# Kernel optimization log

Measured on AMD Instinct MI355X. Metric: run time of the kernel, lower is better.

The kernel has to match this reference:

```python
import jax, jax.numpy as jnp
import numpy as np

B, T, D, H = 2, 2048, 1024, 16
DK = D // H


def setup_inputs() -> dict:
    key = jax.random.key(0)
    ks = jax.random.split(key, 12)
    q = jax.random.normal(ks[0], (B, T, D), jnp.float32)
    k = jax.random.normal(ks[1], (B, T, D), jnp.float32)
    v = jax.random.normal(ks[2], (B, T, D), jnp.float32)
    # padding mask [B,1,T]: 1 = valid, 0 = pad (nonzero per torch eq(0) semantics)
    lengths = jnp.array([T, (3 * T) // 4])
    mask = (jnp.arange(T)[None, None, :] < lengths[:, None, None]).astype(jnp.int32)
    s = 0.02
    Wq = jax.random.normal(ks[3], (D, D), jnp.float32) * s
    Wk = jax.random.normal(ks[4], (D, D), jnp.float32) * s
    Wv = jax.random.normal(ks[5], (D, D), jnp.float32) * s
    Wo = jax.random.normal(ks[6], (D, D), jnp.float32) * s
    bq = jnp.zeros((D,), jnp.float32)
    bk = jnp.zeros((D,), jnp.float32)
    bv = jnp.zeros((D,), jnp.float32)
    bo = jnp.zeros((D,), jnp.float32)
    return {"query": q, "key": k, "value": v, "mask": mask,
            "Wq": Wq, "bq": bq, "Wk": Wk, "bk": bk,
            "Wv": Wv, "bv": bv, "Wo": Wo, "bo": bo}


def reference(query, key, value, mask, Wq, bq, Wk, bk, Wv, bv, Wo, bo):
    # q,k,v projections -> [B, H, T, DK]
    def proj(x, W, b):
        return (x @ W.T + b).reshape(B, T, H, DK).transpose(0, 2, 1, 3)
    q = proj(query, Wq, bq)
    k = proj(key, Wk, bk)
    v = proj(value, Wv, bv)
    scores = jnp.einsum("bhqd,bhkd->bhqk", q, k) * (DK ** -0.5)  # [B,H,T,T]
    m = (mask == 0)[:, None, :, :]  # [B,1,1,T] broadcast over heads/queries
    scores = jnp.where(m, -jnp.inf, scores)
    attn = jax.nn.softmax(scores, axis=-1)
    attn = jnp.where(m, 0.0, attn)
    x = jnp.einsum("bhqk,bhkd->bhqd", attn, v)  # [B,H,T,DK]
    x = x.transpose(0, 2, 1, 3).reshape(B, T, D)
    return x @ Wo.T + bo
```

## Files before the change

### kernel.cpp

```cpp
#include <hip/hip_runtime.h>

typedef unsigned short u16;
typedef unsigned int u32;
typedef __bf16 bf16x8 __attribute__((ext_vector_type(8)));
typedef __bf16 bf16x4 __attribute__((ext_vector_type(4)));
typedef float floatx4 __attribute__((ext_vector_type(4)));

#define BB 2
#define TT 2048
#define DD 1024
#define HH 16
#define DKK 64
#define ACT (BB * TT * DD)
#define WTE (DD * DD)

__device__ inline u16 f2bf(float f) {
    union { float f; u32 u; } c; c.f = f;
    u32 r = (c.u + 0x7fffu + ((c.u >> 16) & 1u)) >> 16;
    return (u16)r;
}
__device__ inline u32 pack2bf(float a, float b) {
    return (u32)f2bf(a) | ((u32)f2bf(b) << 16);
}

typedef __attribute__((address_space(1))) const u32 gas_u32;
typedef __attribute__((address_space(3))) u32 las_u32;
__device__ __forceinline__ void gl2lds16(const u16* g, u16* l) {
    __builtin_amdgcn_global_load_lds((gas_u32*)g, (las_u32*)l, 16, 0, 0);
}

struct CvtArgs { const float* src[7]; u16* dst[7]; };
__global__ __launch_bounds__(256) void convert_bf16(CvtArgs a) {
    int bid = blockIdx.x, t, local;
    if (bid < 768) { t = bid >> 8; local = bid & 255; }
    else { int r = bid - 768; t = 3 + (r >> 6); local = r & 63; }
    const float* s = a.src[t];
    u16* d = a.dst[t];
    const int base = local * 16384;
    for (int i = 0; i < 8; i++) {
        const int idx = base + i * 2048 + threadIdx.x * 8;
        float4 x0 = *(const float4*)(s + idx);
        float4 x1 = *(const float4*)(s + idx + 4);
        uint4 p;
        p.x = pack2bf(x0.x, x0.y); p.y = pack2bf(x0.z, x0.w);
        p.z = pack2bf(x1.x, x1.y); p.w = pack2bf(x1.z, x1.w);
        *(uint4*)(d + idx) = p;
    }
}

__global__ __launch_bounds__(256) void qkv_gemm(
    const u16* __restrict__ Qc, const u16* __restrict__ Kc,
    const u16* __restrict__ Vc,
    const u16* __restrict__ Wqc, const u16* __restrict__ Wkc,
    const u16* __restrict__ Wvc,
    const float* __restrict__ bq, const float* __restrict__ bk,
    const float* __restrict__ bv,
    u16* __restrict__ ws)
{
    __shared__ __align__(16) u16 As[128 * 32];
    __shared__ __align__(16) u16 Bs[128 * 32];
    const int z = blockIdx.z;
    const u16* A = (z == 0) ? Qc : (z == 1) ? Kc : Vc;
    const u16* W = (z == 0) ? Wqc : (z == 1) ? Wkc : Wvc;
    const float* bias = (z == 0) ? bq : (z == 1) ? bk : bv;
    u16* out = ws + (size_t)z * (size_t)BB * HH * TT * DKK;

    const int tid  = threadIdx.x;
    const int wave = tid >> 6, lane = tid & 63;
    const int quad = lane >> 4, l16 = lane & 15;
    const int wm = wave & 1, wn = wave >> 1;
    const int m0 = blockIdx.y * 128, n0 = blockIdx.x * 128;
    const int K = DD;

    const int lrow = lane >> 2, lcol = (lane & 3) * 8;
    const u16* Ag0 = A + (size_t)(m0 + wave * 16 + lrow) * K + lcol;
    const u16* Ag1 = A + (size_t)(m0 + 64 + wave * 16 + lrow) * K + lcol;
    const u16* Wg0 = W + (size_t)(n0 + wave * 16 + lrow) * K + lcol;
    const u16* Wg1 = W + (size_t)(n0 + 64 + wave * 16 + lrow) * K + lcol;
    u16* AsD0 = &As[(wave * 16) * 32];
    u16* AsD1 = &As[(64 + wave * 16) * 32];
    u16* BsD0 = &Bs[(wave * 16) * 32];
    u16* BsD1 = &Bs[(64 + wave * 16) * 32];

    floatx4 acc[4][4];
    for (int i = 0; i < 4; i++)
        for (int j = 0; j < 4; j++)
            acc[i][j] = floatx4{0.f, 0.f, 0.f, 0.f};

    for (int k0 = 0; k0 < K; k0 += 32) {
        __syncthreads();
        gl2lds16(Ag0 + k0, AsD0);
        gl2lds16(Ag1 + k0, AsD1);
        gl2lds16(Wg0 + k0, BsD0);
        gl2lds16(Wg1 + k0, BsD1);
        __syncthreads();

        bf16x8 af[4], bfr[4];
        for (int mi = 0; mi < 4; mi++)
            af[mi] = *(const bf16x8*)&As[(wm * 64 + mi * 16 + l16) * 32 + quad * 8];
        for (int ni = 0; ni < 4; ni++)
            bfr[ni] = *(const bf16x8*)&Bs[(wn * 64 + ni * 16 + l16) * 32 + quad * 8];
        for (int mi = 0; mi < 4; mi++)
            for (int ni = 0; ni < 4; ni++)
                acc[mi][ni] = __builtin_amdgcn_mfma_f32_16x16x32_bf16(
                    af[mi], bfr[ni], acc[mi][ni], 0, 0, 0);
    }

    for (int ni = 0; ni < 4; ni++) {
        const int n = n0 + wn * 64 + ni * 16 + l16;
        const float bv2 = bias[n];
        for (int mi = 0; mi < 4; mi++) {
            for (int vv = 0; vv < 4; vv++) {
                const int m = m0 + wm * 64 + mi * 16 + quad * 4 + vv;
                float val = acc[mi][ni][vv] + bv2;
                if (z == 0) val *= 0.125f;
                const int b = m >> 11, t = m & 2047, h = n >> 6, dk = n & 63;
                if (z == 2) {
                    const int tp = (t & ~63) | ((t >> 4) & 3) | ((t & 15) << 2);
                    out[(((size_t)(b * HH + h)) * DKK + dk) * TT + tp] = f2bf(val);
                } else {
                    out[(((size_t)(b * HH + h)) * TT + t) * DKK + dk] = f2bf(val);
                }
            }
        }
    }
}

__global__ __launch_bounds__(256) void out_gemm(
    const u16* __restrict__ Av, const u16* __restrict__ Wv,
    const float* __restrict__ bias, float* __restrict__ outv)
{
    __shared__ __align__(16) u16 As[128 * 32];
    __shared__ __align__(16) u16 Bs[128 * 32];
    const int tid  = threadIdx.x;
    const int wave = tid >> 6, lane = tid & 63;
    const int quad = lane >> 4, l16 = lane & 15;
    const int wm = wave & 1, wn = wave >> 1;
    const int m0 = blockIdx.y * 128, n0 = blockIdx.x * 128;
    const int K = DD, N = DD;

    const int lrow = lane >> 2, lcol = (lane & 3) * 8;
    const u16* Ag0 = Av + (size_t)(m0 + wave * 16 + lrow) * K + lcol;
    const u16* Ag1 = Av + (size_t)(m0 + 64 + wave * 16 + lrow) * K + lcol;
    const u16* Wg0 = Wv + (size_t)(n0 + wave * 16 + lrow) * K + lcol;
    const u16* Wg1 = Wv + (size_t)(n0 + 64 + wave * 16 + lrow) * K + lcol;
    u16* AsD0 = &As[(wave * 16) * 32];
    u16* AsD1 = &As[(64 + wave * 16) * 32];
    u16* BsD0 = &Bs[(wave * 16) * 32];
    u16* BsD1 = &Bs[(64 + wave * 16) * 32];

    floatx4 acc[4][4];
    for (int i = 0; i < 4; i++)
        for (int j = 0; j < 4; j++)
            acc[i][j] = floatx4{0.f, 0.f, 0.f, 0.f};

    for (int k0 = 0; k0 < K; k0 += 32) {
        __syncthreads();
        gl2lds16(Ag0 + k0, AsD0);
        gl2lds16(Ag1 + k0, AsD1);
        gl2lds16(Wg0 + k0, BsD0);
        gl2lds16(Wg1 + k0, BsD1);
        __syncthreads();

        bf16x8 af[4], bfr[4];
        for (int mi = 0; mi < 4; mi++)
            af[mi] = *(const bf16x8*)&As[(wm * 64 + mi * 16 + l16) * 32 + quad * 8];
        for (int ni = 0; ni < 4; ni++)
            bfr[ni] = *(const bf16x8*)&Bs[(wn * 64 + ni * 16 + l16) * 32 + quad * 8];
        for (int mi = 0; mi < 4; mi++)
            for (int ni = 0; ni < 4; ni++)
                acc[mi][ni] = __builtin_amdgcn_mfma_f32_16x16x32_bf16(
                    af[mi], bfr[ni], acc[mi][ni], 0, 0, 0);
    }

    for (int ni = 0; ni < 4; ni++) {
        const int n = n0 + wn * 64 + ni * 16 + l16;
        const float bv2 = bias[n];
        for (int mi = 0; mi < 4; mi++)
            for (int vv = 0; vv < 4; vv++) {
                const int m = m0 + wm * 64 + mi * 16 + quad * 4 + vv;
                outv[(size_t)m * N + n] = acc[mi][ni][vv] + bv2;
            }
    }
}

__global__ __launch_bounds__(256) void attn_kernel(
    const u16* __restrict__ Qp, const u16* __restrict__ Kp,
    const u16* __restrict__ Vpt, const int* __restrict__ mask,
    u16* __restrict__ Xa)
{
    constexpr int LDK = 72, LDP = 72;
    __shared__ __align__(16) u16 Ks[64 * LDK];
    __shared__ __align__(16) u16 Vs[64 * LDK];
    __shared__ __align__(16) __bf16 Pl[4][32][LDP];
    const int tid  = threadIdx.x;
    const int wave = tid >> 6, lane = tid & 63;
    const int quad = lane >> 4, l16 = lane & 15;
    const int bid = blockIdx.x;
    const int qt = bid & 15, bh = bid >> 4;
    const int b = bh >> 4, h = bh & 15;
    const int qbase = qt * 128 + wave * 32;

    const u16* Qb = Qp + (size_t)bh * TT * DKK;
    const u16* Kb = Kp + (size_t)bh * TT * DKK;
    const u16* Vb = Vpt + (size_t)bh * DKK * TT;
    const int* mk = mask + b * TT;

    const int srow = tid >> 3, scol = (tid & 7) * 8;

    bf16x8 qf[2][2];
    for (int mb = 0; mb < 2; mb++) {
        qf[mb][0] = *(const bf16x8*)&Qb[(size_t)(qbase + mb * 16 + l16) * DKK + quad * 8];
        qf[mb][1] = *(const bf16x8*)&Qb[(size_t)(qbase + mb * 16 + l16) * DKK + 32 + quad * 8];
    }

    floatx4 o[2][4];
    float rsum[2][4];
    for (int mb = 0; mb < 2; mb++)
        for (int i = 0; i < 4; i++) {
            o[mb][i] = floatx4{0.f, 0.f, 0.f, 0.f};
            rsum[mb][i] = 0.f;
        }

    uint4 kr0 = *(const uint4*)&Kb[(size_t)srow * DKK + scol];
    uint4 kr1 = *(const uint4*)&Kb[(size_t)(32 + srow) * DKK + scol];
    uint4 vr0 = *(const uint4*)&Vb[(size_t)srow * TT + scol];
    uint4 vr1 = *(const uint4*)&Vb[(size_t)(32 + srow) * TT + scol];

    for (int ti = 0; ti < TT / 64; ti++) {
        const int k0 = ti * 64;
        __syncthreads();
        *(uint4*)&Ks[srow * LDK + scol] = kr0;
        *(uint4*)&Ks[(32 + srow) * LDK + scol] = kr1;
        *(uint4*)&Vs[srow * LDK + scol] = vr0;
        *(uint4*)&Vs[(32 + srow) * LDK + scol] = vr1;
        __syncthreads();
        if (ti + 1 < TT / 64) {
            kr0 = *(const uint4*)&Kb[(size_t)(k0 + 64 + srow) * DKK + scol];
            kr1 = *(const uint4*)&Kb[(size_t)(k0 + 96 + srow) * DKK + scol];
            vr0 = *(const uint4*)&Vb[(size_t)srow * TT + k0 + 64 + scol];
            vr1 = *(const uint4*)&Vb[(size_t)(32 + srow) * TT + k0 + 64 + scol];
        }

        const int mv0 = mk[k0 + l16];
        const int mv1 = mk[k0 + 16 + l16];
        const int mv2 = mk[k0 + 32 + l16];
        const int mv3 = mk[k0 + 48 + l16];
        if (!__any(mv0 | mv1 | mv2 | mv3)) continue;
        const float mf[4] = { mv0 ? 1.f : 0.f, mv1 ? 1.f : 0.f,
                              mv2 ? 1.f : 0.f, mv3 ? 1.f : 0.f };

        bf16x8 kf[4][2];
        for (int c = 0; c < 4; c++) {
            kf[c][0] = *(const bf16x8*)&Ks[(c * 16 + l16) * LDK + quad * 8];
            kf[c][1] = *(const bf16x8*)&Ks[(c * 16 + l16) * LDK + 32 + quad * 8];
        }

        for (int mb = 0; mb < 2; mb++) {
            floatx4 s[4];
            for (int c = 0; c < 4; c++) s[c] = floatx4{0.f, 0.f, 0.f, 0.f};
            for (int c = 0; c < 4; c++) {
                s[c] = __builtin_amdgcn_mfma_f32_16x16x32_bf16(qf[mb][0], kf[c][0], s[c], 0, 0, 0);
                s[c] = __builtin_amdgcn_mfma_f32_16x16x32_bf16(qf[mb][1], kf[c][1], s[c], 0, 0, 0);
            }
            float p[4][4];
            for (int c = 0; c < 4; c++)
                for (int v = 0; v < 4; v++) {
                    p[c][v] = __expf(s[c][v]) * mf[c];
                    rsum[mb][v] += p[c][v];
                }
            for (int v = 0; v < 4; v++) {
                bf16x4 pv = { (__bf16)p[0][v], (__bf16)p[1][v],
                              (__bf16)p[2][v], (__bf16)p[3][v] };
                *(bf16x4*)&Pl[wave][mb * 16 + quad * 4 + v][l16 * 4] = pv;
            }
        }
        __asm__ volatile("" ::: "memory");
        bf16x8 pf[2][2];
        for (int mb = 0; mb < 2; mb++) {
            pf[mb][0] = *(const bf16x8*)&Pl[wave][mb * 16 + l16][quad * 8];
            pf[mb][1] = *(const bf16x8*)&Pl[wave][mb * 16 + l16][32 + quad * 8];
        }
        __asm__ volatile("" ::: "memory");

        for (int nb = 0; nb < 4; nb++) {
            const bf16x8 vf0 = *(const bf16x8*)&Vs[(nb * 16 + l16) * LDK + quad * 8];
            const bf16x8 vf1 = *(const bf16x8*)&Vs[(nb * 16 + l16) * LDK + 32 + quad * 8];
            o[0][nb] = __builtin_amdgcn_mfma_f32_16x16x32_bf16(pf[0][0], vf0, o[0][nb], 0, 0, 0);
            o[0][nb] = __builtin_amdgcn_mfma_f32_16x16x32_bf16(pf[0][1], vf1, o[0][nb], 0, 0, 0);
            o[1][nb] = __builtin_amdgcn_mfma_f32_16x16x32_bf16(pf[1][0], vf0, o[1][nb], 0, 0, 0);
            o[1][nb] = __builtin_amdgcn_mfma_f32_16x16x32_bf16(pf[1][1], vf1, o[1][nb], 0, 0, 0);
        }
    }

    for (int off = 1; off < 16; off <<= 1)
        for (int mb = 0; mb < 2; mb++)
            for (int v = 0; v < 4; v++)
                rsum[mb][v] += __shfl_xor(rsum[mb][v], off, 64);

    for (int mb = 0; mb < 2; mb++) {
        float inv[4];
        for (int v = 0; v < 4; v++) inv[v] = 1.0f / rsum[mb][v];
        for (int nb = 0; nb < 4; nb++)
            for (int v = 0; v < 4; v++) {
                const int t = qbase + mb * 16 + quad * 4 + v;
                Xa[((size_t)b * TT + t) * DD + h * DKK + nb * 16 + l16] =
                    f2bf(o[mb][nb][v] * inv[v]);
            }
    }
}

extern "C" void kernel_launch(void* const* d_in, const int* in_sizes, int n_in,
                              void* d_out, int out_size, void* d_ws, size_t ws_size,
                              hipStream_t stream) {
    const float* q    = (const float*)d_in[0];
    const float* k    = (const float*)d_in[1];
    const float* v    = (const float*)d_in[2];
    const int*   mask = (const int*)d_in[3];
    const float* Wq   = (const float*)d_in[4];
    const float* bq   = (const float*)d_in[5];
    const float* Wk   = (const float*)d_in[6];
    const float* bk   = (const float*)d_in[7];
    const float* Wv   = (const float*)d_in[8];
    const float* bv   = (const float*)d_in[9];
    const float* Wo   = (const float*)d_in[10];
    const float* bo   = (const float*)d_in[11];

    u16* Qc  = (u16*)d_ws;
    u16* Kc  = Qc + (size_t)ACT;
    u16* Vc  = Kc + (size_t)ACT;
    u16* Wqc = Vc + (size_t)ACT;
    u16* Wkc = Wqc + (size_t)WTE;
    u16* Wvc = Wkc + (size_t)WTE;
    u16* Woc = Wvc + (size_t)WTE;
    u16* Qp  = Woc + (size_t)WTE;
    u16* Kp  = Qp + (size_t)ACT;
    u16* Vpt = Kp + (size_t)ACT;
    u16* Xa  = Vpt + (size_t)ACT;

    CvtArgs ca;
    ca.src[0] = q;  ca.dst[0] = Qc;
    ca.src[1] = k;  ca.dst[1] = Kc;
    ca.src[2] = v;  ca.dst[2] = Vc;
    ca.src[3] = Wq; ca.dst[3] = Wqc;
    ca.src[4] = Wk; ca.dst[4] = Wkc;
    ca.src[5] = Wv; ca.dst[5] = Wvc;
    ca.src[6] = Wo; ca.dst[6] = Woc;
    convert_bf16<<<1024, 256, 0, stream>>>(ca);

    qkv_gemm<<<dim3(DD / 128, (BB * TT) / 128, 3), 256, 0, stream>>>(
        Qc, Kc, Vc, Wqc, Wkc, Wvc, bq, bk, bv, Qp);

    attn_kernel<<<dim3(BB * HH * (TT / 128)), 256, 0, stream>>>(Qp, Kp, Vpt, mask, Xa);

    out_gemm<<<dim3(DD / 128, (BB * TT) / 128), 256, 0, stream>>>(Xa, Woc, bo, (float*)d_out);
}
```

Before: 261.4 us.

## Split attention over key halves with a combine kernel; widen GEMM K-step

The attention kernel now splits the key range into two halves along a second grid dimension. Each half writes unnormalized bf16 partial outputs and row sums into reused workspace, and a new combine kernel adds the halves, normalizes, and writes the head-interleaved activation. This doubles the number of attention blocks, improving CU occupancy and balancing work across the padded batch, at the cost of an extra launch, extra memory traffic for the partials, and bf16 rounding of unnormalized partials. Separately, both GEMMs now stage 64-wide K tiles per barrier pair instead of 32, halving the synchronizations per K and doubling LDS use.

```diff
diff --git a/kernel.cpp b/kernel.cpp
--- a/kernel.cpp
+++ b/kernel.cpp
@@ -13,6 +13,7 @@
 #define DKK 64
 #define ACT (BB * TT * DD)
 #define WTE (DD * DD)
+#define BHT (BB * HH * TT)
 
 __device__ inline u16 f2bf(float f) {
     union { float f; u32 u; } c; c.f = f;
@@ -57,8 +58,8 @@
     const float* __restrict__ bv,
     u16* __restrict__ ws)
 {
-    __shared__ __align__(16) u16 As[128 * 32];
-    __shared__ __align__(16) u16 Bs[128 * 32];
+    __shared__ __align__(16) u16 As[2 * 128 * 32];
+    __shared__ __align__(16) u16 Bs[2 * 128 * 32];
     const int z = blockIdx.z;
     const u16* A = (z == 0) ? Qc : (z == 1) ? Kc : Vc;
     const u16* W = (z == 0) ? Wqc : (z == 1) ? Wkc : Wvc;
@@ -73,37 +74,43 @@
     const int K = DD;
 
     const int lrow = lane >> 2, lcol = (lane & 3) * 8;
-    const u16* Ag0 = A + (size_t)(m0 + wave * 16 + lrow) * K + lcol;
-    const u16* Ag1 = A + (size_t)(m0 + 64 + wave * 16 + lrow) * K + lcol;
-    const u16* Wg0 = W + (size_t)(n0 + wave * 16 + lrow) * K + lcol;
-    const u16* Wg1 = W + (size_t)(n0 + 64 + wave * 16 + lrow) * K + lcol;
-    u16* AsD0 = &As[(wave * 16) * 32];
-    u16* AsD1 = &As[(64 + wave * 16) * 32];
-    u16* BsD0 = &Bs[(wave * 16) * 32];
-    u16* BsD1 = &Bs[(64 + wave * 16) * 32];
+    const u16* Ag[2] = { A + (size_t)(m0 + wave * 16 + lrow) * K + lcol,
+                         A + (size_t)(m0 + 64 + wave * 16 + lrow) * K + lcol };
+    const u16* Wg[2] = { W + (size_t)(n0 + wave * 16 + lrow) * K + lcol,
+                         W + (size_t)(n0 + 64 + wave * 16 + lrow) * K + lcol };
+    u16* AsD[2][2], *BsD[2][2];
+    for (int kh = 0; kh < 2; kh++)
+        for (int j = 0; j < 2; j++) {
+            AsD[kh][j] = &As[kh * 4096 + (j * 64 + wave * 16) * 32];
+            BsD[kh][j] = &Bs[kh * 4096 + (j * 64 + wave * 16) * 32];
+        }
 
     floatx4 acc[4][4];
     for (int i = 0; i < 4; i++)
         for (int j = 0; j < 4; j++)
             acc[i][j] = floatx4{0.f, 0.f, 0.f, 0.f};
 
-    for (int k0 = 0; k0 < K; k0 += 32) {
-        __syncthreads();
-        gl2lds16(Ag0 + k0, AsD0);
-        gl2lds16(Ag1 + k0, AsD1);
-        gl2lds16(Wg0 + k0, BsD0);
-        gl2lds16(Wg1 + k0, BsD1);
-        __syncthreads();
-
-        bf16x8 af[4], bfr[4];
-        for (int mi = 0; mi < 4; mi++)
-            af[mi] = *(const bf16x8*)&As[(wm * 64 + mi * 16 + l16) * 32 + quad * 8];
-        for (int ni = 0; ni < 4; ni++)
-            bfr[ni] = *(const bf16x8*)&Bs[(wn * 64 + ni * 16 + l16) * 32 + quad * 8];
-        for (int mi = 0; mi < 4; mi++)
+    for (int k0 = 0; k0 < K; k0 += 64) {
+        __syncthreads();
+        for (int kh = 0; kh < 2; kh++)
+            for (int j = 0; j < 2; j++) {
+                gl2lds16(Ag[j] + k0 + kh * 32, AsD[kh][j]);
+                gl2lds16(Wg[j] + k0 + kh * 32, BsD[kh][j]);
+            }
+        __syncthreads();
+
+        bf16x8 af[4][2], bfr[4][2];
+        for (int kh = 0; kh < 2; kh++) {
+            for (int mi = 0; mi < 4; mi++)
+                af[mi][kh] = *(const bf16x8*)&As[kh * 4096 + (wm * 64 + mi * 16 + l16) * 32 + quad * 8];
             for (int ni = 0; ni < 4; ni++)
-                acc[mi][ni] = __builtin_amdgcn_mfma_f32_16x16x32_bf16(
-                    af[mi], bfr[ni], acc[mi][ni], 0, 0, 0);
+                bfr[ni][kh] = *(const bf16x8*)&Bs[kh * 4096 + (wn * 64 + ni * 16 + l16) * 32 + quad * 8];
+        }
+        for (int kh = 0; kh < 2; kh++)
+            for (int mi = 0; mi < 4; mi++)
+                for (int ni = 0; ni < 4; ni++)
+                    acc[mi][ni] = __builtin_amdgcn_mfma_f32_16x16x32_bf16(
+                        af[mi][kh], bfr[ni][kh], acc[mi][ni], 0, 0, 0);
     }
 
     for (int ni = 0; ni < 4; ni++) {
@@ -130,8 +137,8 @@
     const u16* __restrict__ Av, const u16* __restrict__ Wv,
     const float* __restrict__ bias, float* __restrict__ outv)
 {
-    __shared__ __align__(16) u16 As[128 * 32];
-    __shared__ __align__(16) u16 Bs[128 * 32];
+    __shared__ __align__(16) u16 As[2 * 128 * 32];
+    __shared__ __align__(16) u16 Bs[2 * 128 * 32];
     const int tid  = threadIdx.x;
     const int wave = tid >> 6, lane = tid & 63;
     const int quad = lane >> 4, l16 = lane & 15;
@@ -140,37 +147,43 @@
     const int K = DD, N = DD;
 
     const int lrow = lane >> 2, lcol = (lane & 3) * 8;
-    const u16* Ag0 = Av + (size_t)(m0 + wave * 16 + lrow) * K + lcol;
-    const u16* Ag1 = Av + (size_t)(m0 + 64 + wave * 16 + lrow) * K + lcol;
-    const u16* Wg0 = Wv + (size_t)(n0 + wave * 16 + lrow) * K + lcol;
-    const u16* Wg1 = Wv + (size_t)(n0 + 64 + wave * 16 + lrow) * K + lcol;
-    u16* AsD0 = &As[(wave * 16) * 32];
-    u16* AsD1 = &As[(64 + wave * 16) * 32];
-    u16* BsD0 = &Bs[(wave * 16) * 32];
-    u16* BsD1 = &Bs[(64 + wave * 16) * 32];
+    const u16* Ag[2] = { Av + (size_t)(m0 + wave * 16 + lrow) * K + lcol,
+                         Av + (size_t)(m0 + 64 + wave * 16 + lrow) * K + lcol };
+    const u16* Wg[2] = { Wv + (size_t)(n0 + wave * 16 + lrow) * K + lcol,
+                         Wv + (size_t)(n0 + 64 + wave * 16 + lrow) * K + lcol };
+    u16* AsD[2][2], *BsD[2][2];
+    for (int kh = 0; kh < 2; kh++)
+        for (int j = 0; j < 2; j++) {
+            AsD[kh][j] = &As[kh * 4096 + (j * 64 + wave * 16) * 32];
+            BsD[kh][j] = &Bs[kh * 4096 + (j * 64 + wave * 16) * 32];
+        }
 
     floatx4 acc[4][4];
     for (int i = 0; i < 4; i++)
         for (int j = 0; j < 4; j++)
             acc[i][j] = floatx4{0.f, 0.f, 0.f, 0.f};
 
-    for (int k0 = 0; k0 < K; k0 += 32) {
-        __syncthreads();
-        gl2lds16(Ag0 + k0, AsD0);
-        gl2lds16(Ag1 + k0, AsD1);
-        gl2lds16(Wg0 + k0, BsD0);
-        gl2lds16(Wg1 + k0, BsD1);
-        __syncthreads();
-
-        bf16x8 af[4], bfr[4];
-        for (int mi = 0; mi < 4; mi++)
-            af[mi] = *(const bf16x8*)&As[(wm * 64 + mi * 16 + l16) * 32 + quad * 8];
-        for (int ni = 0; ni < 4; ni++)
-            bfr[ni] = *(const bf16x8*)&Bs[(wn * 64 + ni * 16 + l16) * 32 + quad * 8];
-        for (int mi = 0; mi < 4; mi++)
+    for (int k0 = 0; k0 < K; k0 += 64) {
+        __syncthreads();
+        for (int kh = 0; kh < 2; kh++)
+            for (int j = 0; j < 2; j++) {
+                gl2lds16(Ag[j] + k0 + kh * 32, AsD[kh][j]);
+                gl2lds16(Wg[j] + k0 + kh * 32, BsD[kh][j]);
+            }
+        __syncthreads();
+
+        bf16x8 af[4][2], bfr[4][2];
+        for (int kh = 0; kh < 2; kh++) {
+            for (int mi = 0; mi < 4; mi++)
+                af[mi][kh] = *(const bf16x8*)&As[kh * 4096 + (wm * 64 + mi * 16 + l16) * 32 + quad * 8];
             for (int ni = 0; ni < 4; ni++)
-                acc[mi][ni] = __builtin_amdgcn_mfma_f32_16x16x32_bf16(
-                    af[mi], bfr[ni], acc[mi][ni], 0, 0, 0);
+                bfr[ni][kh] = *(const bf16x8*)&Bs[kh * 4096 + (wn * 64 + ni * 16 + l16) * 32 + quad * 8];
+        }
+        for (int kh = 0; kh < 2; kh++)
+            for (int mi = 0; mi < 4; mi++)
+                for (int ni = 0; ni < 4; ni++)
+                    acc[mi][ni] = __builtin_amdgcn_mfma_f32_16x16x32_bf16(
+                        af[mi][kh], bfr[ni][kh], acc[mi][ni], 0, 0, 0);
     }
 
     for (int ni = 0; ni < 4; ni++) {
@@ -187,7 +200,7 @@
 __global__ __launch_bounds__(256) void attn_kernel(
     const u16* __restrict__ Qp, const u16* __restrict__ Kp,
     const u16* __restrict__ Vpt, const int* __restrict__ mask,
-    u16* __restrict__ Xa)
+    u16* __restrict__ Opart, float* __restrict__ Rpart)
 {
     constexpr int LDK = 72, LDP = 72;
     __shared__ __align__(16) u16 Ks[64 * LDK];
@@ -197,9 +210,11 @@
     const int wave = tid >> 6, lane = tid & 63;
     const int quad = lane >> 4, l16 = lane & 15;
     const int bid = blockIdx.x;
+    const int half = blockIdx.y;
     const int qt = bid & 15, bh = bid >> 4;
-    const int b = bh >> 4, h = bh & 15;
+    const int b = bh >> 4;
     const int qbase = qt * 128 + wave * 32;
+    const int kstart = half * (TT / 2);
 
     const u16* Qb = Qp + (size_t)bh * TT * DKK;
     const u16* Kb = Kp + (size_t)bh * TT * DKK;
@@ -222,20 +237,20 @@
             rsum[mb][i] = 0.f;
         }
 
-    uint4 kr0 = *(const uint4*)&Kb[(size_t)srow * DKK + scol];
-    uint4 kr1 = *(const uint4*)&Kb[(size_t)(32 + srow) * DKK + scol];
-    uint4 vr0 = *(const uint4*)&Vb[(size_t)srow * TT + scol];
-    uint4 vr1 = *(const uint4*)&Vb[(size_t)(32 + srow) * TT + scol];
-
-    for (int ti = 0; ti < TT / 64; ti++) {
-        const int k0 = ti * 64;
+    uint4 kr0 = *(const uint4*)&Kb[(size_t)(kstart + srow) * DKK + scol];
+    uint4 kr1 = *(const uint4*)&Kb[(size_t)(kstart + 32 + srow) * DKK + scol];
+    uint4 vr0 = *(const uint4*)&Vb[(size_t)srow * TT + kstart + scol];
+    uint4 vr1 = *(const uint4*)&Vb[(size_t)(32 + srow) * TT + kstart + scol];
+
+    for (int ti = 0; ti < TT / 128; ti++) {
+        const int k0 = kstart + ti * 64;
         __syncthreads();
         *(uint4*)&Ks[srow * LDK + scol] = kr0;
         *(uint4*)&Ks[(32 + srow) * LDK + scol] = kr1;
         *(uint4*)&Vs[srow * LDK + scol] = vr0;
         *(uint4*)&Vs[(32 + srow) * LDK + scol] = vr1;
         __syncthreads();
-        if (ti + 1 < TT / 64) {
+        if (ti + 1 < TT / 128) {
             kr0 = *(const uint4*)&Kb[(size_t)(k0 + 64 + srow) * DKK + scol];
             kr1 = *(const uint4*)&Kb[(size_t)(k0 + 96 + srow) * DKK + scol];
             vr0 = *(const uint4*)&Vb[(size_t)srow * TT + k0 + 64 + scol];
@@ -298,16 +313,38 @@
             for (int v = 0; v < 4; v++)
                 rsum[mb][v] += __shfl_xor(rsum[mb][v], off, 64);
 
+    u16* Ob = Opart + (size_t)half * BHT * DKK + (size_t)bh * TT * DKK;
+    float* Rb = Rpart + (size_t)half * BHT + (size_t)bh * TT;
     for (int mb = 0; mb < 2; mb++) {
-        float inv[4];
-        for (int v = 0; v < 4; v++) inv[v] = 1.0f / rsum[mb][v];
         for (int nb = 0; nb < 4; nb++)
             for (int v = 0; v < 4; v++) {
-                const int t = qbase + mb * 16 + quad * 4 + v;
-                Xa[((size_t)b * TT + t) * DD + h * DKK + nb * 16 + l16] =
-                    f2bf(o[mb][nb][v] * inv[v]);
-            }
-    }
+                const int r = qbase + mb * 16 + quad * 4 + v;
+                Ob[(size_t)r * DKK + nb * 16 + l16] = f2bf(o[mb][nb][v]);
+            }
+        if (l16 == 0)
+            for (int v = 0; v < 4; v++)
+                Rb[qbase + mb * 16 + quad * 4 + v] = rsum[mb][v];
+    }
+}
+
+__global__ __launch_bounds__(256) void attn_combine(
+    const u16* __restrict__ Opart, const float* __restrict__ Rpart,
+    u16* __restrict__ Xa)
+{
+    const int g = blockIdx.x * 256 + threadIdx.x;
+    const int row = g >> 3, cg = g & 7;
+    const int bh = row >> 11, t = row & 2047;
+    const int b = bh >> 4, h = bh & 15;
+    const bf16x8 o0 = *(const bf16x8*)&Opart[(size_t)row * DKK + cg * 8];
+    const bf16x8 o1 = *(const bf16x8*)&Opart[(size_t)BHT * DKK + (size_t)row * DKK + cg * 8];
+    const float inv = 1.0f / (Rpart[row] + Rpart[BHT + row]);
+    float r[8];
+    for (int i = 0; i < 8; i++)
+        r[i] = ((float)o0[i] + (float)o1[i]) * inv;
+    uint4 p;
+    p.x = pack2bf(r[0], r[1]); p.y = pack2bf(r[2], r[3]);
+    p.z = pack2bf(r[4], r[5]); p.w = pack2bf(r[6], r[7]);
+    *(uint4*)&Xa[(((size_t)b * TT + t) * DD) + h * DKK + cg * 8] = p;
 }
 
 extern "C" void kernel_launch(void* const* d_in, const int* in_sizes, int n_in,
@@ -338,6 +375,9 @@
     u16* Vpt = Kp + (size_t)ACT;
     u16* Xa  = Vpt + (size_t)ACT;
 
+    u16*   Opart = Qc;
+    float* Rpart = (float*)Vc;
+
     CvtArgs ca;
     ca.src[0] = q;  ca.dst[0] = Qc;
     ca.src[1] = k;  ca.dst[1] = Kc;
@@ -351,7 +391,10 @@
     qkv_gemm<<<dim3(DD / 128, (BB * TT) / 128, 3), 256, 0, stream>>>(
         Qc, Kc, Vc, Wqc, Wkc, Wvc, bq, bk, bv, Qp);
 
-    attn_kernel<<<dim3(BB * HH * (TT / 128)), 256, 0, stream>>>(Qp, Kp, Vpt, mask, Xa);
+    attn_kernel<<<dim3(BB * HH * (TT / 128), 2), 256, 0, stream>>>(
+        Qp, Kp, Vpt, mask, Opart, Rpart);
+
+    attn_combine<<<(BHT * 8) / 256, 256, 0, stream>>>(Opart, Rpart, Xa);
 
     out_gemm<<<dim3(DD / 128, (BB * TT) / 128), 256, 0, stream>>>(Xa, Woc, bo, (float*)d_out);
 }
```

Result: faster. 255.7 us (-2.2%).
